# Kernel optimization log

Measured on AMD Instinct MI355X. Metric: run time of the kernel, lower is better.

The kernel has to match this reference:

```python
import jax, jax.numpy as jnp
import numpy as np

MARGIN = 0.5  # init kwarg margin=0.5 (float -> fix_margin branch)

N, D, NUM_CLASSES = 8192, 128, 512


def setup_inputs() -> dict:
    key = jax.random.key(0)
    k1, k2 = jax.random.split(key)
    embeds = jax.random.normal(k1, (N, D), dtype=jnp.float32)
    labels = jax.random.randint(k2, (N,), 0, NUM_CLASSES)
    return {"embeds": embeds, "labels": labels}


def reference(embeds, labels):
    n = embeds.shape[0]
    # --- batch-hard mining (detached in original: .detach().cpu().numpy()) ---
    # Euclidean pairwise distances via Gram trick (avoids [N,N,D] intermediate).
    sq = jnp.sum(embeds * embeds, axis=1)  # [N]
    d2 = sq[:, None] + sq[None, :] - 2.0 * (embeds @ embeds.T)  # [N,N]
    dist = jnp.sqrt(jnp.maximum(d2, 0.0))
    dist = jax.lax.stop_gradient(dist)

    same = labels[:, None] == labels[None, :]  # [N,N]
    eye = jnp.eye(n, dtype=bool)
    pos_mask = same & ~eye          # same label, not self
    neg_mask = ~same                # different label (diag excluded since same there)

    pos_idx = jnp.argmax(jnp.where(pos_mask, dist, -jnp.inf), axis=1)  # hardest positive
    neg_idx = jnp.argmin(jnp.where(neg_mask, dist, jnp.inf), axis=1)   # hardest negative

    # --- margin loss with metric='sqeuclidean' (gradients flow through gathers) ---
    dp = embeds - embeds[pos_idx]
    dn = embeds - embeds[neg_idx]
    ap = jnp.sum(dp * dp, axis=1)
    an = jnp.sum(dn * dn, axis=1)
    return jnp.mean(jax.nn.relu(ap - an + MARGIN))
```

## Files before the change

### kernel.cpp

```cpp
#include <hip/hip_runtime.h>
#include <stdint.h>

#define NROWS 8192
#define DIM 128
#define ROWB 256
#define NIBLK 32
#define NCHUNK 32
#define MARGIN 0.5f

typedef short short8 __attribute__((ext_vector_type(8)));
typedef float f32x4 __attribute__((ext_vector_type(4)));
typedef int   int4v __attribute__((ext_vector_type(4)));

#define GLDS16(g, l) __builtin_amdgcn_global_load_lds( \
    (const __attribute__((address_space(1))) unsigned int*)(g), \
    (__attribute__((address_space(3))) unsigned int*)(l), 16, 0, 0)

static __device__ __forceinline__ unsigned short f2bf(float f) {
    union { float f; unsigned u; } x; x.f = f;
    unsigned u = x.u;
    return (unsigned short)((u + 0x7FFFu + ((u >> 16) & 1u)) >> 16);
}

__global__ __launch_bounds__(256) void prep(const float* __restrict__ emb,
                                            unsigned short* __restrict__ e16,
                                            float* __restrict__ cbuf) {
    const int lane = threadIdx.x & 63;
    const int row = blockIdx.x * 4 + (threadIdx.x >> 6);
    const float2 v = reinterpret_cast<const float2*>(emb + row * DIM)[lane];
    float sq = v.x * v.x + v.y * v.y;
#pragma unroll
    for (int m = 1; m < 64; m <<= 1) sq += __shfl_xor(sq, m, 64);
    const unsigned pack = ((unsigned)f2bf(v.y) << 16) | (unsigned)f2bf(v.x);
    *reinterpret_cast<unsigned*>(e16 + row * DIM + lane * 2) = pack;
    if (lane == 0) cbuf[row] = sq + 512.0f;
}

__global__ __launch_bounds__(256) void mine(const unsigned short* __restrict__ e16,
                                            const float* __restrict__ cbuf,
                                            const int* __restrict__ labels,
                                            unsigned* __restrict__ pos_part,
                                            unsigned* __restrict__ neg_part) {
    __shared__ char smem[2][16384];
    const int tid  = threadIdx.x;
    const int wave = tid >> 6;
    const int lane = tid & 63;
    const int l15  = lane & 15;
    const int lhi  = lane >> 4;
    const int iblk = blockIdx.x & (NIBLK - 1);
    const int cblk = blockIdx.x / NIBLK;
    const int ibase = iblk * 256 + wave * 64;
    const char* e8 = (const char*)e16;
    const int jcbase = cblk * 256;

    {
        const char* gs = e8 + (size_t)(jcbase + wave * 16) * ROWB;
        char* lb = &smem[0][wave * 4096];
#pragma unroll
        for (int q = 0; q < 4; ++q) {
            const int r16 = q * 4 + lhi;
            const int ch  = l15 ^ r16;
            GLDS16(gs + r16 * ROWB + ch * 16, lb + q * 1024);
        }
    }

    short8 bfrag[4][4];
    int labi[4];
#pragma unroll
    for (int it = 0; it < 4; ++it) {
        const int row = ibase + it * 16 + l15;
#pragma unroll
        for (int ks = 0; ks < 4; ++ks)
            bfrag[it][ks] = *reinterpret_cast<const short8*>(e8 + (size_t)row * ROWB + ks * 64 + lhi * 16);
        labi[it] = labels[row];
    }

    unsigned bp[4] = {0u, 0u, 0u, 0u};
    unsigned bn[4] = {0xFFFFFFFFu, 0xFFFFFFFFu, 0xFFFFFFFFu, 0xFFFFFFFFu};

    __syncthreads();

#pragma unroll
    for (int st = 0; st < 4; ++st) {
        if (st < 3) {
            const char* gs = e8 + (size_t)(jcbase + (st + 1) * 64 + wave * 16) * ROWB;
            char* lb = &smem[(st + 1) & 1][wave * 4096];
#pragma unroll
            for (int q = 0; q < 4; ++q) {
                const int r16 = q * 4 + lhi;
                const int ch  = l15 ^ r16;
                GLDS16(gs + r16 * ROWB + ch * 16, lb + q * 1024);
            }
        }
        const char* buf = smem[st & 1];
#pragma unroll
        for (int sub = 0; sub < 4; ++sub) {
            const int jb = jcbase + st * 64 + sub * 16;
            const int4v labj = *reinterpret_cast<const int4v*>(labels + jb + lhi * 4);
            const f32x4 c4   = *reinterpret_cast<const f32x4*>(cbuf + jb + lhi * 4);
            const f32x4 cinit = c4 * -0.5f;

            short8 af[4];
#pragma unroll
            for (int ks = 0; ks < 4; ++ks)
                af[ks] = *reinterpret_cast<const short8*>(
                    buf + (sub * 16 + l15) * ROWB + ((ks * 4 + lhi) ^ l15) * 16);

            f32x4 acc[4];
#pragma unroll
            for (int it = 0; it < 4; ++it)
                acc[it] = __builtin_amdgcn_mfma_f32_16x16x32_bf16(af[0], bfrag[it][0], cinit, 0, 0, 0);
#pragma unroll
            for (int ks = 1; ks < 4; ++ks)
#pragma unroll
                for (int it = 0; it < 4; ++it)
                    acc[it] = __builtin_amdgcn_mfma_f32_16x16x32_bf16(af[ks], bfrag[it][ks], acc[it], 0, 0, 0);

            const int j0 = jb + lhi * 4;
#pragma unroll
            for (int it = 0; it < 4; ++it) {
#pragma unroll
                for (int r = 0; r < 4; ++r) {
                    union { float f; unsigned u; } cv; cv.f = acc[it][r];
                    const unsigned cand = (cv.u & 0xFFFFE000u) | (unsigned)(j0 + r);
                    const bool eq = (labj[r] == labi[it]);
                    const unsigned psel = eq ? cand : 0u;
                    const unsigned nsel = eq ? 0xFFFFFFFFu : cand;
                    bp[it] = bp[it] > psel ? bp[it] : psel;
                    bn[it] = bn[it] < nsel ? bn[it] : nsel;
                }
            }
        }
        __syncthreads();
    }

#pragma unroll
    for (int it = 0; it < 4; ++it) {
        unsigned p = bp[it], n = bn[it];
        unsigned o;
        o = (unsigned)__shfl_xor((int)p, 16, 64); p = p > o ? p : o;
        o = (unsigned)__shfl_xor((int)p, 32, 64); p = p > o ? p : o;
        o = (unsigned)__shfl_xor((int)n, 16, 64); n = n < o ? n : o;
        o = (unsigned)__shfl_xor((int)n, 32, 64); n = n < o ? n : o;
        if (lane < 16) {
            pos_part[cblk * NROWS + ibase + it * 16 + lane] = p;
            neg_part[cblk * NROWS + ibase + it * 16 + lane] = n;
        }
    }
}

__global__ __launch_bounds__(256) void lossk(const float* __restrict__ emb,
                                             const unsigned* __restrict__ pos_part,
                                             const unsigned* __restrict__ neg_part,
                                             float* __restrict__ bsum) {
    __shared__ float wsum[4];
    const int tid = threadIdx.x, lane = tid & 63, wave = tid >> 6;
    const int i = blockIdx.x * 4 + wave;
    const int c = lane & 31;
    unsigned v = (lane < 32) ? pos_part[c * NROWS + i] : ~neg_part[c * NROWS + i];
#pragma unroll
    for (int m = 1; m < 32; m <<= 1) {
        const unsigned o = (unsigned)__shfl_xor((int)v, m, 64);
        v = v > o ? v : o;
    }
    const unsigned o32 = (unsigned)__shfl_xor((int)v, 32, 64);
    const unsigned pmax = (lane < 32) ? v : o32;
    const unsigned nmin = ~((lane < 32) ? o32 : v);
    const int jp = (int)(pmax & 8191u);
    const int jn = (int)(nmin & 8191u);
    const float2 a = reinterpret_cast<const float2*>(emb + (size_t)i  * DIM)[lane];
    const float2 b = reinterpret_cast<const float2*>(emb + (size_t)jp * DIM)[lane];
    const float2 cc = reinterpret_cast<const float2*>(emb + (size_t)jn * DIM)[lane];
    float dx = a.x - b.x, dy = a.y - b.y;
    const float ap = dx * dx + dy * dy;
    dx = a.x - cc.x; dy = a.y - cc.y;
    const float an = dx * dx + dy * dy;
    float s = ap - an;
#pragma unroll
    for (int m = 1; m < 64; m <<= 1) s += __shfl_xor(s, m, 64);
    if (lane == 0) wsum[wave] = fmaxf(s + MARGIN, 0.f);
    __syncthreads();
    if (tid == 0) bsum[blockIdx.x] = wsum[0] + wsum[1] + wsum[2] + wsum[3];
}

__global__ __launch_bounds__(256) void fin(const float* __restrict__ bsum,
                                           float* __restrict__ out) {
    __shared__ float wsum[4];
    const int tid = threadIdx.x, lane = tid & 63, wave = tid >> 6;
    float s = 0.f;
#pragma unroll
    for (int k = 0; k < 8; ++k) s += bsum[tid + k * 256];
#pragma unroll
    for (int m = 1; m < 64; m <<= 1) s += __shfl_xor(s, m, 64);
    if (lane == 0) wsum[wave] = s;
    __syncthreads();
    if (tid == 0) out[0] = (wsum[0] + wsum[1] + wsum[2] + wsum[3]) * (1.0f / (float)NROWS);
}

extern "C" void kernel_launch(void* const* d_in, const int* in_sizes, int n_in,
                              void* d_out, int out_size, void* d_ws, size_t ws_size,
                              hipStream_t stream) {
    const float* emb   = (const float*)d_in[0];
    const int* labels  = (const int*)d_in[1];
    float* out = (float*)d_out;
    char* ws = (char*)d_ws;

    unsigned short* e16 = (unsigned short*)ws;
    float* cbuf         = (float*)(ws + (size_t)2097152);
    unsigned* pos_part  = (unsigned*)(ws + (size_t)2097152 + 32768);
    unsigned* neg_part  = pos_part + (size_t)NCHUNK * NROWS;
    float* bsum         = (float*)(neg_part + (size_t)NCHUNK * NROWS);

    prep<<<2048, 256, 0, stream>>>(emb, e16, cbuf);
    mine<<<NIBLK * NCHUNK, 256, 0, stream>>>(e16, cbuf, labels, pos_part, neg_part);
    lossk<<<2048, 256, 0, stream>>>(emb, pos_part, neg_part, bsum);
    fin<<<1, 256, 0, stream>>>(bsum, out);
}
```

Measured before the change: 97.70 us.

## Double column-chunk split in mining and replace final reduce kernel with atomics

Splits the column range of the mining kernel into 64 chunks of 128 columns instead of 32 chunks of 256. This doubles the grid to 2048 blocks and halves shared memory per block, which should improve occupancy and load balance across CUs. The loss kernel now reduces 64 partials per row using all lanes and accumulates the mean with a float atomicAdd. That removes the separate final reduction kernel launch. In exchange it doubles the partial-result traffic, makes the summation order nondeterministic, and needs the output zeroed in the prep kernel.

```diff
diff --git a/kernel.cpp b/kernel.cpp
--- a/kernel.cpp
+++ b/kernel.cpp
@@ -5,7 +5,7 @@
 #define DIM 128
 #define ROWB 256
 #define NIBLK 32
-#define NCHUNK 32
+#define NCHUNK 64
 #define MARGIN 0.5f
 
 typedef short short8 __attribute__((ext_vector_type(8)));
@@ -24,7 +24,8 @@
 
 __global__ __launch_bounds__(256) void prep(const float* __restrict__ emb,
                                             unsigned short* __restrict__ e16,
-                                            float* __restrict__ cbuf) {
+                                            float* __restrict__ cbuf,
+                                            float* __restrict__ out) {
     const int lane = threadIdx.x & 63;
     const int row = blockIdx.x * 4 + (threadIdx.x >> 6);
     const float2 v = reinterpret_cast<const float2*>(emb + row * DIM)[lane];
@@ -34,6 +35,7 @@
     const unsigned pack = ((unsigned)f2bf(v.y) << 16) | (unsigned)f2bf(v.x);
     *reinterpret_cast<unsigned*>(e16 + row * DIM + lane * 2) = pack;
     if (lane == 0) cbuf[row] = sq + 512.0f;
+    if (blockIdx.x == 0 && threadIdx.x == 0) out[0] = 0.0f;
 }
 
 __global__ __launch_bounds__(256) void mine(const unsigned short* __restrict__ e16,
@@ -41,7 +43,7 @@
                                             const int* __restrict__ labels,
                                             unsigned* __restrict__ pos_part,
                                             unsigned* __restrict__ neg_part) {
-    __shared__ char smem[2][16384];
+    __shared__ char smem[2][8192];
     const int tid  = threadIdx.x;
     const int wave = tid >> 6;
     const int lane = tid & 63;
@@ -51,16 +53,16 @@
     const int cblk = blockIdx.x / NIBLK;
     const int ibase = iblk * 256 + wave * 64;
     const char* e8 = (const char*)e16;
-    const int jcbase = cblk * 256;
+    const int jcbase = cblk * 128;
 
     {
-        const char* gs = e8 + (size_t)(jcbase + wave * 16) * ROWB;
-        char* lb = &smem[0][wave * 4096];
-#pragma unroll
-        for (int q = 0; q < 4; ++q) {
-            const int r16 = q * 4 + lhi;
-            const int ch  = l15 ^ r16;
-            GLDS16(gs + r16 * ROWB + ch * 16, lb + q * 1024);
+        const char* gs = e8 + (size_t)(jcbase + wave * 8) * ROWB;
+        char* lb = &smem[0][wave * 2048];
+#pragma unroll
+        for (int q = 0; q < 2; ++q) {
+            const int r = wave * 8 + q * 4 + lhi;
+            const int ch = l15 ^ (r & 15);
+            GLDS16(gs + (q * 4 + lhi) * ROWB + ch * 16, lb + q * 1024);
         }
     }
 
@@ -83,19 +85,19 @@
 #pragma unroll
     for (int st = 0; st < 4; ++st) {
         if (st < 3) {
-            const char* gs = e8 + (size_t)(jcbase + (st + 1) * 64 + wave * 16) * ROWB;
-            char* lb = &smem[(st + 1) & 1][wave * 4096];
-#pragma unroll
-            for (int q = 0; q < 4; ++q) {
-                const int r16 = q * 4 + lhi;
-                const int ch  = l15 ^ r16;
-                GLDS16(gs + r16 * ROWB + ch * 16, lb + q * 1024);
+            const char* gs = e8 + (size_t)(jcbase + (st + 1) * 32 + wave * 8) * ROWB;
+            char* lb = &smem[(st + 1) & 1][wave * 2048];
+#pragma unroll
+            for (int q = 0; q < 2; ++q) {
+                const int r = wave * 8 + q * 4 + lhi;
+                const int ch = l15 ^ (r & 15);
+                GLDS16(gs + (q * 4 + lhi) * ROWB + ch * 16, lb + q * 1024);
             }
         }
         const char* buf = smem[st & 1];
 #pragma unroll
-        for (int sub = 0; sub < 4; ++sub) {
-            const int jb = jcbase + st * 64 + sub * 16;
+        for (int sub = 0; sub < 2; ++sub) {
+            const int jb = jcbase + st * 32 + sub * 16;
             const int4v labj = *reinterpret_cast<const int4v*>(labels + jb + lhi * 4);
             const f32x4 c4   = *reinterpret_cast<const f32x4*>(cbuf + jb + lhi * 4);
             const f32x4 cinit = c4 * -0.5f;
@@ -152,49 +154,35 @@
 __global__ __launch_bounds__(256) void lossk(const float* __restrict__ emb,
                                              const unsigned* __restrict__ pos_part,
                                              const unsigned* __restrict__ neg_part,
-                                             float* __restrict__ bsum) {
+                                             float* __restrict__ out) {
     __shared__ float wsum[4];
     const int tid = threadIdx.x, lane = tid & 63, wave = tid >> 6;
     const int i = blockIdx.x * 4 + wave;
-    const int c = lane & 31;
-    unsigned v = (lane < 32) ? pos_part[c * NROWS + i] : ~neg_part[c * NROWS + i];
-#pragma unroll
-    for (int m = 1; m < 32; m <<= 1) {
-        const unsigned o = (unsigned)__shfl_xor((int)v, m, 64);
-        v = v > o ? v : o;
-    }
-    const unsigned o32 = (unsigned)__shfl_xor((int)v, 32, 64);
-    const unsigned pmax = (lane < 32) ? v : o32;
-    const unsigned nmin = ~((lane < 32) ? o32 : v);
-    const int jp = (int)(pmax & 8191u);
-    const int jn = (int)(nmin & 8191u);
+    unsigned p = pos_part[lane * NROWS + i];
+    unsigned n = neg_part[lane * NROWS + i];
+#pragma unroll
+    for (int m = 1; m < 64; m <<= 1) {
+        const unsigned op = (unsigned)__shfl_xor((int)p, m, 64);
+        const unsigned on = (unsigned)__shfl_xor((int)n, m, 64);
+        p = p > op ? p : op;
+        n = n < on ? n : on;
+    }
+    const int jp = (int)(p & 8191u);
+    const int jn = (int)(n & 8191u);
     const float2 a = reinterpret_cast<const float2*>(emb + (size_t)i  * DIM)[lane];
     const float2 b = reinterpret_cast<const float2*>(emb + (size_t)jp * DIM)[lane];
-    const float2 cc = reinterpret_cast<const float2*>(emb + (size_t)jn * DIM)[lane];
+    const float2 c = reinterpret_cast<const float2*>(emb + (size_t)jn * DIM)[lane];
     float dx = a.x - b.x, dy = a.y - b.y;
     const float ap = dx * dx + dy * dy;
-    dx = a.x - cc.x; dy = a.y - cc.y;
+    dx = a.x - c.x; dy = a.y - c.y;
     const float an = dx * dx + dy * dy;
     float s = ap - an;
 #pragma unroll
     for (int m = 1; m < 64; m <<= 1) s += __shfl_xor(s, m, 64);
     if (lane == 0) wsum[wave] = fmaxf(s + MARGIN, 0.f);
     __syncthreads();
-    if (tid == 0) bsum[blockIdx.x] = wsum[0] + wsum[1] + wsum[2] + wsum[3];
-}
-
-__global__ __launch_bounds__(256) void fin(const float* __restrict__ bsum,
-                                           float* __restrict__ out) {
-    __shared__ float wsum[4];
-    const int tid = threadIdx.x, lane = tid & 63, wave = tid >> 6;
-    float s = 0.f;
-#pragma unroll
-    for (int k = 0; k < 8; ++k) s += bsum[tid + k * 256];
-#pragma unroll
-    for (int m = 1; m < 64; m <<= 1) s += __shfl_xor(s, m, 64);
-    if (lane == 0) wsum[wave] = s;
-    __syncthreads();
-    if (tid == 0) out[0] = (wsum[0] + wsum[1] + wsum[2] + wsum[3]) * (1.0f / (float)NROWS);
+    if (tid == 0)
+        atomicAdd(out, (wsum[0] + wsum[1] + wsum[2] + wsum[3]) * (1.0f / (float)NROWS));
 }
 
 extern "C" void kernel_launch(void* const* d_in, const int* in_sizes, int n_in,
@@ -209,10 +197,8 @@
     float* cbuf         = (float*)(ws + (size_t)2097152);
     unsigned* pos_part  = (unsigned*)(ws + (size_t)2097152 + 32768);
     unsigned* neg_part  = pos_part + (size_t)NCHUNK * NROWS;
-    float* bsum         = (float*)(neg_part + (size_t)NCHUNK * NROWS);
-
-    prep<<<2048, 256, 0, stream>>>(emb, e16, cbuf);
+
+    prep<<<2048, 256, 0, stream>>>(emb, e16, cbuf, out);
     mine<<<NIBLK * NCHUNK, 256, 0, stream>>>(e16, cbuf, labels, pos_part, neg_part);
-    lossk<<<2048, 256, 0, stream>>>(emb, pos_part, neg_part, bsum);
-    fin<<<1, 256, 0, stream>>>(bsum, out);
-}
+    lossk<<<2048, 256, 0, stream>>>(emb, pos_part, neg_part, out);
+}
```

New measurement: 126.1 us. 1.29x slower.

## Shrink per-wave row tile, use 512-thread blocks and atomic min/max reduction

Applied to the files above, without the earlier changes.

The mining kernel now gives each wave 16 query rows instead of 64, uses 512-thread blocks over 128 rows, and doubles the number of row blocks. The per-chunk partial arrays are dropped: results go straight into global atomicMax/atomicMin on per-row packed keys, which prep initialises. The loss kernel then reads one value per row instead of reducing 32 partials. The aim is more waves and occupancy plus less partial-buffer traffic, at the cost of less register reuse of the column tile per MFMA and atomic contention.

```diff
diff --git a/kernel.cpp b/kernel.cpp
--- a/kernel.cpp
+++ b/kernel.cpp
@@ -4,7 +4,7 @@
 #define NROWS 8192
 #define DIM 128
 #define ROWB 256
-#define NIBLK 32
+#define NIBLK 64
 #define NCHUNK 32
 #define MARGIN 0.5f
 
@@ -24,7 +24,10 @@
 
 __global__ __launch_bounds__(256) void prep(const float* __restrict__ emb,
                                             unsigned short* __restrict__ e16,
-                                            float* __restrict__ cbuf) {
+                                            float* __restrict__ cbuf,
+                                            unsigned* __restrict__ pos,
+                                            unsigned* __restrict__ neg,
+                                            float* __restrict__ out) {
     const int lane = threadIdx.x & 63;
     const int row = blockIdx.x * 4 + (threadIdx.x >> 6);
     const float2 v = reinterpret_cast<const float2*>(emb + row * DIM)[lane];
@@ -34,13 +37,16 @@
     const unsigned pack = ((unsigned)f2bf(v.y) << 16) | (unsigned)f2bf(v.x);
     *reinterpret_cast<unsigned*>(e16 + row * DIM + lane * 2) = pack;
     if (lane == 0) cbuf[row] = sq + 512.0f;
-}
-
-__global__ __launch_bounds__(256) void mine(const unsigned short* __restrict__ e16,
-                                            const float* __restrict__ cbuf,
-                                            const int* __restrict__ labels,
-                                            unsigned* __restrict__ pos_part,
-                                            unsigned* __restrict__ neg_part) {
+    if (lane == 1) pos[row] = 0u;
+    if (lane == 2) neg[row] = 0xFFFFFFFFu;
+    if (blockIdx.x == 0 && threadIdx.x == 0) out[0] = 0.0f;
+}
+
+__global__ __launch_bounds__(512, 6) void mine(const unsigned short* __restrict__ e16,
+                                               const float* __restrict__ cbuf,
+                                               const int* __restrict__ labels,
+                                               unsigned* __restrict__ pos,
+                                               unsigned* __restrict__ neg) {
     __shared__ char smem[2][16384];
     const int tid  = threadIdx.x;
     const int wave = tid >> 6;
@@ -49,53 +55,49 @@
     const int lhi  = lane >> 4;
     const int iblk = blockIdx.x & (NIBLK - 1);
     const int cblk = blockIdx.x / NIBLK;
-    const int ibase = iblk * 256 + wave * 64;
+    const int irow = iblk * 128 + wave * 16 + l15;
     const char* e8 = (const char*)e16;
-    const int jcbase = cblk * 256;
+    const int jc = cblk * 256;
 
     {
-        const char* gs = e8 + (size_t)(jcbase + wave * 16) * ROWB;
-        char* lb = &smem[0][wave * 4096];
-#pragma unroll
-        for (int q = 0; q < 4; ++q) {
-            const int r16 = q * 4 + lhi;
-            const int ch  = l15 ^ r16;
-            GLDS16(gs + r16 * ROWB + ch * 16, lb + q * 1024);
+        const char* gs = e8 + (size_t)jc * ROWB;
+        char* lb = smem[0];
+#pragma unroll
+        for (int q = 0; q < 2; ++q) {
+            const int r = q * 32 + (tid >> 4);
+            const int d = tid & 15;
+            const int g = d ^ (r & 15);
+            GLDS16(gs + (size_t)r * ROWB + g * 16, lb + q * 8192 + tid * 16);
         }
     }
 
-    short8 bfrag[4][4];
-    int labi[4];
-#pragma unroll
-    for (int it = 0; it < 4; ++it) {
-        const int row = ibase + it * 16 + l15;
-#pragma unroll
-        for (int ks = 0; ks < 4; ++ks)
-            bfrag[it][ks] = *reinterpret_cast<const short8*>(e8 + (size_t)row * ROWB + ks * 64 + lhi * 16);
-        labi[it] = labels[row];
-    }
-
-    unsigned bp[4] = {0u, 0u, 0u, 0u};
-    unsigned bn[4] = {0xFFFFFFFFu, 0xFFFFFFFFu, 0xFFFFFFFFu, 0xFFFFFFFFu};
+    short8 bfrag[4];
+#pragma unroll
+    for (int ks = 0; ks < 4; ++ks)
+        bfrag[ks] = *reinterpret_cast<const short8*>(e8 + (size_t)irow * ROWB + (ks * 4 + lhi) * 16);
+    const int labi = labels[irow];
+
+    unsigned bp = 0u, bn = 0xFFFFFFFFu;
 
     __syncthreads();
 
 #pragma unroll
     for (int st = 0; st < 4; ++st) {
         if (st < 3) {
-            const char* gs = e8 + (size_t)(jcbase + (st + 1) * 64 + wave * 16) * ROWB;
-            char* lb = &smem[(st + 1) & 1][wave * 4096];
-#pragma unroll
-            for (int q = 0; q < 4; ++q) {
-                const int r16 = q * 4 + lhi;
-                const int ch  = l15 ^ r16;
-                GLDS16(gs + r16 * ROWB + ch * 16, lb + q * 1024);
+            const char* gs = e8 + (size_t)(jc + (st + 1) * 64) * ROWB;
+            char* lb = smem[(st + 1) & 1];
+#pragma unroll
+            for (int q = 0; q < 2; ++q) {
+                const int r = q * 32 + (tid >> 4);
+                const int d = tid & 15;
+                const int g = d ^ (r & 15);
+                GLDS16(gs + (size_t)r * ROWB + g * 16, lb + q * 8192 + tid * 16);
             }
         }
         const char* buf = smem[st & 1];
 #pragma unroll
-        for (int sub = 0; sub < 4; ++sub) {
-            const int jb = jcbase + st * 64 + sub * 16;
+        for (int jt = 0; jt < 4; ++jt) {
+            const int jb = jc + st * 64 + jt * 16;
             const int4v labj = *reinterpret_cast<const int4v*>(labels + jb + lhi * 4);
             const f32x4 c4   = *reinterpret_cast<const f32x4*>(cbuf + jb + lhi * 4);
             const f32x4 cinit = c4 * -0.5f;
@@ -104,76 +106,57 @@
 #pragma unroll
             for (int ks = 0; ks < 4; ++ks)
                 af[ks] = *reinterpret_cast<const short8*>(
-                    buf + (sub * 16 + l15) * ROWB + ((ks * 4 + lhi) ^ l15) * 16);
-
-            f32x4 acc[4];
-#pragma unroll
-            for (int it = 0; it < 4; ++it)
-                acc[it] = __builtin_amdgcn_mfma_f32_16x16x32_bf16(af[0], bfrag[it][0], cinit, 0, 0, 0);
+                    buf + (jt * 16 + l15) * ROWB + (((ks * 4 + lhi) ^ l15) * 16));
+
+            f32x4 acc = __builtin_amdgcn_mfma_f32_16x16x32_bf16(af[0], bfrag[0], cinit, 0, 0, 0);
 #pragma unroll
             for (int ks = 1; ks < 4; ++ks)
-#pragma unroll
-                for (int it = 0; it < 4; ++it)
-                    acc[it] = __builtin_amdgcn_mfma_f32_16x16x32_bf16(af[ks], bfrag[it][ks], acc[it], 0, 0, 0);
+                acc = __builtin_amdgcn_mfma_f32_16x16x32_bf16(af[ks], bfrag[ks], acc, 0, 0, 0);
 
             const int j0 = jb + lhi * 4;
 #pragma unroll
-            for (int it = 0; it < 4; ++it) {
-#pragma unroll
-                for (int r = 0; r < 4; ++r) {
-                    union { float f; unsigned u; } cv; cv.f = acc[it][r];
-                    const unsigned cand = (cv.u & 0xFFFFE000u) | (unsigned)(j0 + r);
-                    const bool eq = (labj[r] == labi[it]);
-                    const unsigned psel = eq ? cand : 0u;
-                    const unsigned nsel = eq ? 0xFFFFFFFFu : cand;
-                    bp[it] = bp[it] > psel ? bp[it] : psel;
-                    bn[it] = bn[it] < nsel ? bn[it] : nsel;
-                }
+            for (int r = 0; r < 4; ++r) {
+                union { float f; unsigned u; } cv; cv.f = acc[r];
+                const unsigned cand = (cv.u & 0xFFFFE000u) | (unsigned)(j0 + r);
+                const bool eq = (labj[r] == labi);
+                const unsigned psel = eq ? cand : 0u;
+                const unsigned nsel = eq ? 0xFFFFFFFFu : cand;
+                bp = bp > psel ? bp : psel;
+                bn = bn < nsel ? bn : nsel;
             }
         }
         __syncthreads();
     }
 
-#pragma unroll
-    for (int it = 0; it < 4; ++it) {
-        unsigned p = bp[it], n = bn[it];
+    {
         unsigned o;
-        o = (unsigned)__shfl_xor((int)p, 16, 64); p = p > o ? p : o;
-        o = (unsigned)__shfl_xor((int)p, 32, 64); p = p > o ? p : o;
-        o = (unsigned)__shfl_xor((int)n, 16, 64); n = n < o ? n : o;
-        o = (unsigned)__shfl_xor((int)n, 32, 64); n = n < o ? n : o;
-        if (lane < 16) {
-            pos_part[cblk * NROWS + ibase + it * 16 + lane] = p;
-            neg_part[cblk * NROWS + ibase + it * 16 + lane] = n;
-        }
+        o = (unsigned)__shfl_xor((int)bp, 16, 64); bp = bp > o ? bp : o;
+        o = (unsigned)__shfl_xor((int)bp, 32, 64); bp = bp > o ? bp : o;
+        o = (unsigned)__shfl_xor((int)bn, 16, 64); bn = bn < o ? bn : o;
+        o = (unsigned)__shfl_xor((int)bn, 32, 64); bn = bn < o ? bn : o;
+    }
+    if (lane < 16) {
+        const int i = iblk * 128 + wave * 16 + lane;
+        atomicMax(&pos[i], bp);
+        atomicMin(&neg[i], bn);
     }
 }
 
 __global__ __launch_bounds__(256) void lossk(const float* __restrict__ emb,
-                                             const unsigned* __restrict__ pos_part,
-                                             const unsigned* __restrict__ neg_part,
+                                             const unsigned* __restrict__ pos,
+                                             const unsigned* __restrict__ neg,
                                              float* __restrict__ bsum) {
     __shared__ float wsum[4];
     const int tid = threadIdx.x, lane = tid & 63, wave = tid >> 6;
     const int i = blockIdx.x * 4 + wave;
-    const int c = lane & 31;
-    unsigned v = (lane < 32) ? pos_part[c * NROWS + i] : ~neg_part[c * NROWS + i];
-#pragma unroll
-    for (int m = 1; m < 32; m <<= 1) {
-        const unsigned o = (unsigned)__shfl_xor((int)v, m, 64);
-        v = v > o ? v : o;
-    }
-    const unsigned o32 = (unsigned)__shfl_xor((int)v, 32, 64);
-    const unsigned pmax = (lane < 32) ? v : o32;
-    const unsigned nmin = ~((lane < 32) ? o32 : v);
-    const int jp = (int)(pmax & 8191u);
-    const int jn = (int)(nmin & 8191u);
+    const int jp = (int)(pos[i] & 8191u);
+    const int jn = (int)(neg[i] & 8191u);
     const float2 a = reinterpret_cast<const float2*>(emb + (size_t)i  * DIM)[lane];
     const float2 b = reinterpret_cast<const float2*>(emb + (size_t)jp * DIM)[lane];
-    const float2 cc = reinterpret_cast<const float2*>(emb + (size_t)jn * DIM)[lane];
+    const float2 c = reinterpret_cast<const float2*>(emb + (size_t)jn * DIM)[lane];
     float dx = a.x - b.x, dy = a.y - b.y;
     const float ap = dx * dx + dy * dy;
-    dx = a.x - cc.x; dy = a.y - cc.y;
+    dx = a.x - c.x; dy = a.y - c.y;
     const float an = dx * dx + dy * dy;
     float s = ap - an;
 #pragma unroll
@@ -207,12 +190,12 @@
 
     unsigned short* e16 = (unsigned short*)ws;
     float* cbuf         = (float*)(ws + (size_t)2097152);
-    unsigned* pos_part  = (unsigned*)(ws + (size_t)2097152 + 32768);
-    unsigned* neg_part  = pos_part + (size_t)NCHUNK * NROWS;
-    float* bsum         = (float*)(neg_part + (size_t)NCHUNK * NROWS);
-
-    prep<<<2048, 256, 0, stream>>>(emb, e16, cbuf);
-    mine<<<NIBLK * NCHUNK, 256, 0, stream>>>(e16, cbuf, labels, pos_part, neg_part);
-    lossk<<<2048, 256, 0, stream>>>(emb, pos_part, neg_part, bsum);
+    unsigned* pos       = (unsigned*)(ws + (size_t)2097152 + 32768);
+    unsigned* neg       = pos + NROWS;
+    float* bsum         = (float*)(neg + NROWS);
+
+    prep<<<2048, 256, 0, stream>>>(emb, e16, cbuf, pos, neg, out);
+    mine<<<NIBLK * NCHUNK, 512, 0, stream>>>(e16, cbuf, labels, pos, neg);
+    lossk<<<2048, 256, 0, stream>>>(emb, pos, neg, bsum);
     fin<<<1, 256, 0, stream>>>(bsum, out);
 }
```

New measurement: 94.39 us. -3.4%, faster.
